# Optimization experiments

Hardware: AMD Instinct MI355X
Metric: run time of the kernel (lower is better)

The kernel has to match this reference:

```python
import jax, jax.numpy as jnp
import numpy as np

N_NODE = 50000
N_EDGE = 800000
D = 64       # in_dim = out_dim = hidden_dim
A = 64       # attn_dim
N_REL = 475  # 2*237+1 relation ids
B = 32       # batch of queries


def setup_inputs() -> dict:
    key = jax.random.key(0)
    ks = jax.random.split(key, 16)
    hidden = jax.random.normal(ks[0], (N_NODE, D), dtype=jnp.float32)
    sub = jax.random.randint(ks[1], (N_EDGE,), 0, N_NODE)
    rel = jax.random.randint(ks[2], (N_EDGE,), 0, N_REL)
    obj = jax.random.randint(ks[3], (N_EDGE,), 0, N_NODE)
    edges = jnp.stack([sub, rel, obj], axis=1)  # [E, 3]
    gnn_emb_rel = jax.random.normal(ks[4], (N_REL, D), dtype=jnp.float32)
    mapping = jax.random.randint(ks[5], (N_REL,), 0, N_REL)  # rel id -> unique-rel row
    q_rel = jax.random.randint(ks[6], (B,), 0, N_REL)
    r_idx = jax.random.randint(ks[7], (N_EDGE,), 0, B)  # edge -> query index
    s = 1.0 / np.sqrt(D)
    sa = 1.0 / np.sqrt(A)
    u = lambda k, shape, b: jax.random.uniform(k, shape, jnp.float32, minval=-b, maxval=b)
    return {
        "hidden": hidden,
        "edges": edges,
        "gnn_emb_rel": gnn_emb_rel,
        "mapping": mapping,
        "q_rel": q_rel,
        "r_idx": r_idx,
        "n_node": N_NODE,
        "Ws_w": u(ks[8], (A, D), s),
        "Wr_w": u(ks[9], (A, D), s),
        "Wqr_w": u(ks[10], (A, D), s),
        "Wqr_b": u(ks[11], (A,), s),
        "walpha_w": u(ks[12], (1, A), sa),
        "walpha_b": u(ks[13], (1,), sa),
        "Wh_w": u(ks[14], (D, D), s),
    }


def reference(hidden, edges, gnn_emb_rel, mapping, q_rel, r_idx, n_node,
              Ws_w, Wr_w, Wqr_w, Wqr_b, walpha_w, walpha_b, Wh_w):
    sub, rel, obj = edges[:, 0], edges[:, 1], edges[:, 2]
    hs = hidden[sub]                       # [E, D] gather
    hr = gnn_emb_rel[mapping[rel]]         # [E, D] gather
    # per-query h_qr projected once, then gathered per edge (same math, cheaper)
    hq = gnn_emb_rel[mapping[q_rel]]       # [B, D]
    qr_attn = hq @ Wqr_w.T + Wqr_b         # [B, A]
    pre = hs @ Ws_w.T + hr @ Wr_w.T + qr_attn[r_idx]   # [E, A]
    alpha = jax.nn.sigmoid(jax.nn.relu(pre) @ walpha_w.T + walpha_b)  # [E, 1]
    message = alpha * (hs * hr)            # [E, D]
    message_agg = jax.ops.segment_sum(message, obj, num_segments=n_node)  # [N, D]
    hidden_new = jax.nn.relu(message_agg @ Wh_w.T)  # act = ReLU from GNN_auto
    return hidden_new
```

## Files before the change

### kernel.cpp

```cpp
#include <hip/hip_runtime.h>
#include <hip/hip_bf16.h>

#define D64 64
#define WTP 65
#define LPAD 68

typedef __attribute__((ext_vector_type(8))) short short8;
typedef __attribute__((ext_vector_type(4))) float f32x4;

__device__ inline float lane_bcast(float v, int l) {
    return __uint_as_float(__builtin_amdgcn_readlane(__float_as_uint(v), l));
}
__device__ inline float bf16_lo(unsigned u) { return __uint_as_float(u << 16); }
__device__ inline float bf16_hi(unsigned u) { return __uint_as_float(u & 0xFFFF0000u); }
__device__ inline float bf16u(unsigned short u) { return __uint_as_float((unsigned)u << 16); }
__device__ inline unsigned short f2bf(float f) {
    __hip_bfloat16 b = __float2bfloat16(f);
    return *(unsigned short*)&b;
}

__global__ void cvtW_kernel(const float* __restrict__ W, unsigned short* __restrict__ WsB) {
    int i = blockIdx.x * blockDim.x + threadIdx.x;
    if (i < D64 * D64) WsB[i] = f2bf(W[i]);
}

__global__ void rowmm_mfma_kernel(const float* __restrict__ in,
                                  const unsigned short* __restrict__ WsB,
                                  unsigned short* __restrict__ outb,
                                  unsigned short* __restrict__ inb, int nrows,
                                  const int* __restrict__ edges, const int* __restrict__ r_idx,
                                  int* __restrict__ counts, uint2* __restrict__ epack, int E) {
    __shared__ unsigned short ldsA[4][16 * LPAD];
    __shared__ unsigned short ldsD[4][16 * LPAD];
    int tid = threadIdx.x;
    int lane = tid & 63;
    int wv = tid >> 6;
    int wid = (blockIdx.x * blockDim.x + tid) >> 6;
    int rbase = wid * 16;

    if (rbase < nrows) {
        short8 bfrag[8];
#pragma unroll
        for (int t = 0; t < 4; ++t)
#pragma unroll
            for (int kk = 0; kk < 2; ++kk)
                bfrag[t * 2 + kk] = *(const short8*)(WsB + (size_t)(t * 16 + (lane & 15)) * D64 +
                                                     kk * 32 + (lane >> 4) * 8);

        unsigned short* la = &ldsA[wv][0];
#pragma unroll
        for (int rr = 0; rr < 16; ++rr) {
            int r = rbase + rr;
            float v = (r < nrows) ? in[(size_t)r * D64 + lane] : 0.f;
            la[rr * LPAD + lane] = f2bf(v);
        }
#pragma unroll
        for (int h = 0; h < 2; ++h) {
            int row = h * 8 + (lane >> 3);
            int col8 = (lane & 7) * 8;
            if (rbase + row < nrows) {
                uint4 v = *(const uint4*)(la + row * LPAD + col8);
                *(uint4*)(inb + (size_t)(rbase + row) * D64 + col8) = v;
            }
        }

        f32x4 acc[4];
#pragma unroll
        for (int t = 0; t < 4; ++t) acc[t] = (f32x4){0.f, 0.f, 0.f, 0.f};
#pragma unroll
        for (int kk = 0; kk < 2; ++kk) {
            short8 afrag = *(const short8*)(la + (lane & 15) * LPAD + kk * 32 + (lane >> 4) * 8);
#pragma unroll
            for (int t = 0; t < 4; ++t)
                acc[t] = __builtin_amdgcn_mfma_f32_16x16x32_bf16(afrag, bfrag[t * 2 + kk],
                                                                 acc[t], 0, 0, 0);
        }
        unsigned short* ld = &ldsD[wv][0];
#pragma unroll
        for (int t = 0; t < 4; ++t)
#pragma unroll
            for (int reg = 0; reg < 4; ++reg)
                ld[((lane >> 4) * 4 + reg) * LPAD + t * 16 + (lane & 15)] = f2bf(acc[t][reg]);
#pragma unroll
        for (int h = 0; h < 2; ++h) {
            int row = h * 8 + (lane >> 3);
            int col8 = (lane & 7) * 8;
            if (rbase + row < nrows) {
                uint4 v = *(const uint4*)(ld + row * LPAD + col8);
                *(uint4*)(outb + (size_t)(rbase + row) * D64 + col8) = v;
            }
        }
    }

    int gt = blockIdx.x * blockDim.x + tid;
    int gs = gridDim.x * blockDim.x;
    for (int i = gt; i < E; i += gs) {
        int sub = edges[i * 3 + 0];
        int rel = edges[i * 3 + 1];
        int obj = edges[i * 3 + 2];
        int ri  = r_idx[i];
        epack[i] = make_uint2((unsigned)sub | ((unsigned)rel << 17) | ((unsigned)ri << 26),
                              (unsigned)obj);
        atomicAdd(&counts[obj], 1);
    }
}

__global__ void prep_kernel(const float* __restrict__ emb, const int* __restrict__ mapping,
                            const int* __restrict__ q_rel,
                            const float* __restrict__ Wr, const float* __restrict__ Wqr,
                            const float* __restrict__ Wqr_b,
                            unsigned short* __restrict__ hrmapb,
                            unsigned short* __restrict__ hrWb,
                            unsigned short* __restrict__ qrb, int nrel, int nq) {
    int b = blockIdx.x;
    int lane = threadIdx.x;
    if (b < nrel) {
        int m = mapping[b];
        float v = emb[m * D64 + lane];
        hrmapb[b * D64 + lane] = f2bf(v);
        float acc = 0.f;
#pragma unroll
        for (int d = 0; d < D64; ++d)
            acc = fmaf(lane_bcast(v, d), Wr[lane * D64 + d], acc);
        hrWb[b * D64 + lane] = f2bf(acc);
    } else {
        int q = b - nrel;
        if (q < nq) {
            int m = mapping[q_rel[q]];
            float v = emb[m * D64 + lane];
            float acc = Wqr_b[lane];
#pragma unroll
            for (int d = 0; d < D64; ++d)
                acc = fmaf(lane_bcast(v, d), Wqr[lane * D64 + d], acc);
            qrb[q * D64 + lane] = f2bf(acc);
        }
    }
}

__global__ void scan1_kernel(const int* __restrict__ counts, int* __restrict__ offs,
                             int* __restrict__ partials, int n) {
    __shared__ int tsum[256];
    int t = threadIdx.x;
    int base = blockIdx.x * 1024 + t * 4;
    int v[4];
    int s = 0;
#pragma unroll
    for (int i = 0; i < 4; ++i) {
        int idx = base + i;
        int c = (idx < n) ? counts[idx] : 0;
        v[i] = s;
        s += c;
    }
    tsum[t] = s;
    __syncthreads();
    for (int off = 1; off < 256; off <<= 1) {
        int y = (t >= off) ? tsum[t - off] : 0;
        __syncthreads();
        tsum[t] += y;
        __syncthreads();
    }
    int incl = tsum[t];
    int thread_prefix = incl - s;
    if (t == 255) partials[blockIdx.x] = incl;
#pragma unroll
    for (int i = 0; i < 4; ++i) {
        int idx = base + i;
        if (idx < n) offs[idx] = thread_prefix + v[i];
    }
}

__global__ void scan2_kernel(int* partials, int nb) {
    int t = threadIdx.x;
    int own = (t < nb) ? partials[t] : 0;
    int v = own;
    for (int off = 1; off < 64; off <<= 1) {
        int y = __shfl_up(v, off, 64);
        if (t >= off) v += y;
    }
    if (t < nb) partials[t] = v - own;
}

__global__ void scan3_kernel(int* __restrict__ offs, const int* __restrict__ partials, int n) {
    int base = blockIdx.x * 1024 + threadIdx.x;
    int add = partials[blockIdx.x];
#pragma unroll
    for (int i = 0; i < 4; ++i) {
        int idx = base + i * 256;
        if (idx < n) offs[idx] += add;
    }
}

__global__ void alpha_scatter_kernel(const uint2* __restrict__ epack,
                                     const unsigned short* __restrict__ hsWb,
                                     const unsigned short* __restrict__ hrWb,
                                     const unsigned short* __restrict__ qrb,
                                     const float* __restrict__ walpha_w,
                                     const float* __restrict__ walpha_b,
                                     int* __restrict__ offs, int2* __restrict__ rec,
                                     int E, int half) {
    int tid = blockIdx.x * blockDim.x + threadIdx.x;
    int e0 = tid >> 3;
    int l = tid & 7;
    if (e0 >= half) return;
    int e1 = e0 + half;
    bool has1 = (e1 < E);

    uint2 p0 = epack[e0];
    uint2 p1 = has1 ? epack[e1] : make_uint2(0u, 0u);
    int sub0 = p0.x & 0x1FFFF, rel0 = (p0.x >> 17) & 0x1FF, ri0 = p0.x >> 26, obj0 = (int)p0.y;
    int sub1 = p1.x & 0x1FFFF, rel1 = (p1.x >> 17) & 0x1FF, ri1 = p1.x >> 26, obj1 = (int)p1.y;

    uint4 hv0 = *(const uint4*)(hsWb + (size_t)sub0 * D64 + l * 8);
    uint4 rv0 = *(const uint4*)(hrWb + (size_t)rel0 * D64 + l * 8);
    uint4 qv0 = *(const uint4*)(qrb  + (size_t)ri0  * D64 + l * 8);
    uint4 hv1 = *(const uint4*)(hsWb + (size_t)sub1 * D64 + l * 8);
    uint4 rv1 = *(const uint4*)(hrWb + (size_t)rel1 * D64 + l * 8);
    uint4 qv1 = *(const uint4*)(qrb  + (size_t)ri1  * D64 + l * 8);
    const float4* w = (const float4*)(walpha_w + l * 8);
    float4 w0 = w[0], w1 = w[1];

    float x0, x1;
    x0 = fmaxf(bf16_lo(hv0.x) + bf16_lo(rv0.x) + bf16_lo(qv0.x), 0.f) * w0.x;
    x0 = fmaf(fmaxf(bf16_hi(hv0.x) + bf16_hi(rv0.x) + bf16_hi(qv0.x), 0.f), w0.y, x0);
    x0 = fmaf(fmaxf(bf16_lo(hv0.y) + bf16_lo(rv0.y) + bf16_lo(qv0.y), 0.f), w0.z, x0);
    x0 = fmaf(fmaxf(bf16_hi(hv0.y) + bf16_hi(rv0.y) + bf16_hi(qv0.y), 0.f), w0.w, x0);
    x0 = fmaf(fmaxf(bf16_lo(hv0.z) + bf16_lo(rv0.z) + bf16_lo(qv0.z), 0.f), w1.x, x0);
    x0 = fmaf(fmaxf(bf16_hi(hv0.z) + bf16_hi(rv0.z) + bf16_hi(qv0.z), 0.f), w1.y, x0);
    x0 = fmaf(fmaxf(bf16_lo(hv0.w) + bf16_lo(rv0.w) + bf16_lo(qv0.w), 0.f), w1.z, x0);
    x0 = fmaf(fmaxf(bf16_hi(hv0.w) + bf16_hi(rv0.w) + bf16_hi(qv0.w), 0.f), w1.w, x0);

    x1 = fmaxf(bf16_lo(hv1.x) + bf16_lo(rv1.x) + bf16_lo(qv1.x), 0.f) * w0.x;
    x1 = fmaf(fmaxf(bf16_hi(hv1.x) + bf16_hi(rv1.x) + bf16_hi(qv1.x), 0.f), w0.y, x1);
    x1 = fmaf(fmaxf(bf16_lo(hv1.y) + bf16_lo(rv1.y) + bf16_lo(qv1.y), 0.f), w0.z, x1);
    x1 = fmaf(fmaxf(bf16_hi(hv1.y) + bf16_hi(rv1.y) + bf16_hi(qv1.y), 0.f), w0.w, x1);
    x1 = fmaf(fmaxf(bf16_lo(hv1.z) + bf16_lo(rv1.z) + bf16_lo(qv1.z), 0.f), w1.x, x1);
    x1 = fmaf(fmaxf(bf16_hi(hv1.z) + bf16_hi(rv1.z) + bf16_hi(qv1.z), 0.f), w1.y, x1);
    x1 = fmaf(fmaxf(bf16_lo(hv1.w) + bf16_lo(rv1.w) + bf16_lo(qv1.w), 0.f), w1.z, x1);
    x1 = fmaf(fmaxf(bf16_hi(hv1.w) + bf16_hi(rv1.w) + bf16_hi(qv1.w), 0.f), w1.w, x1);

    x0 += __shfl_xor(x0, 4, 64);
    x1 += __shfl_xor(x1, 4, 64);
    x0 += __shfl_xor(x0, 2, 64);
    x1 += __shfl_xor(x1, 2, 64);
    x0 += __shfl_xor(x0, 1, 64);
    x1 += __shfl_xor(x1, 1, 64);

    if (l == 0) {
        float wb = walpha_b[0];
        float a0 = 1.f / (1.f + __expf(-(x0 + wb)));
        int slot0 = atomicAdd(&offs[obj0], 1);
        rec[slot0] = make_int2(sub0 | (rel0 << 17), __float_as_int(a0));
        if (has1) {
            float a1 = 1.f / (1.f + __expf(-(x1 + wb)));
            int slot1 = atomicAdd(&offs[obj1], 1);
            rec[slot1] = make_int2(sub1 | (rel1 << 17), __float_as_int(a1));
        }
    }
}

__global__ void agg_wh_kernel(const int2* __restrict__ rec, const int* __restrict__ endoff,
                              const unsigned short* __restrict__ hiddenb,
                              const unsigned short* __restrict__ hrmapb,
                              const float* __restrict__ Wh,
                              float* __restrict__ out, int NN) {
    __shared__ float WT[D64 * WTP];
    int tid = threadIdx.x;
    for (int i = tid; i < D64 * D64; i += blockDim.x)
        WT[(i & 63) * WTP + (i >> 6)] = Wh[i];
    __syncthreads();
    int lane = tid & 63;
    int n = (blockIdx.x * blockDim.x + tid) >> 6;
    if (n >= NN) return;
    int start = (n == 0) ? 0 : endoff[n - 1];
    int end = endoff[n];
    start = __builtin_amdgcn_readfirstlane(start);
    end = __builtin_amdgcn_readfirstlane(end);
    float acc0 = 0.f, acc1 = 0.f, acc2 = 0.f, acc3 = 0.f;
    for (int base = start; base < end; base += 64) {
        int cnt = end - base;
        if (cnt > 64) cnt = 64;
        int rx = 0, ry = 0;
        if (lane < cnt) {
            int2 r = rec[base + lane];
            rx = r.x; ry = r.y;
        }
        int j = 0;
        for (; j + 3 < cnt; j += 4) {
            int rx0 = __builtin_amdgcn_readlane(rx, j);
            int ry0 = __builtin_amdgcn_readlane(ry, j);
            int rx1 = __builtin_amdgcn_readlane(rx, j + 1);
            int ry1 = __builtin_amdgcn_readlane(ry, j + 1);
            int rx2 = __builtin_amdgcn_readlane(rx, j + 2);
            int ry2 = __builtin_amdgcn_readlane(ry, j + 2);
            int rx3 = __builtin_amdgcn_readlane(rx, j + 3);
            int ry3 = __builtin_amdgcn_readlane(ry, j + 3);
            float h0 = bf16u(hiddenb[(size_t)(rx0 & 0x1FFFF) * D64 + lane]);
            float m0 = bf16u(hrmapb[(size_t)((unsigned)rx0 >> 17) * D64 + lane]);
            float h1 = bf16u(hiddenb[(size_t)(rx1 & 0x1FFFF) * D64 + lane]);
            float m1 = bf16u(hrmapb[(size_t)((unsigned)rx1 >> 17) * D64 + lane]);
            float h2 = bf16u(hiddenb[(size_t)(rx2 & 0x1FFFF) * D64 + lane]);
            float m2 = bf16u(hrmapb[(size_t)((unsigned)rx2 >> 17) * D64 + lane]);
            float h3 = bf16u(hiddenb[(size_t)(rx3 & 0x1FFFF) * D64 + lane]);
            float m3 = bf16u(hrmapb[(size_t)((unsigned)rx3 >> 17) * D64 + lane]);
            acc0 = fmaf(__uint_as_float(ry0) * h0, m0, acc0);
            acc1 = fmaf(__uint_as_float(ry1) * h1, m1, acc1);
            acc2 = fmaf(__uint_as_float(ry2) * h2, m2, acc2);
            acc3 = fmaf(__uint_as_float(ry3) * h3, m3, acc3);
        }
        for (; j < cnt; ++j) {
            int rx0 = __builtin_amdgcn_readlane(rx, j);
            int ry0 = __builtin_amdgcn_readlane(ry, j);
            float h0 = bf16u(hiddenb[(size_t)(rx0 & 0x1FFFF) * D64 + lane]);
            float m0 = bf16u(hrmapb[(size_t)((unsigned)rx0 >> 17) * D64 + lane]);
            acc0 = fmaf(__uint_as_float(ry0) * h0, m0, acc0);
        }
    }
    float acc = (acc0 + acc1) + (acc2 + acc3);
    float o = 0.f;
#pragma unroll
    for (int d = 0; d < D64; ++d)
        o = fmaf(lane_bcast(acc, d), WT[d * WTP + lane], o);
    out[(size_t)n * D64 + lane] = fmaxf(o, 0.f);
}

extern "C" void kernel_launch(void* const* d_in, const int* in_sizes, int n_in,
                              void* d_out, int out_size, void* d_ws, size_t ws_size,
                              hipStream_t stream) {
    const float* hidden   = (const float*)d_in[0];
    const int*   edges    = (const int*)d_in[1];
    const float* emb_rel  = (const float*)d_in[2];
    const int*   mapping  = (const int*)d_in[3];
    const int*   q_rel    = (const int*)d_in[4];
    const int*   r_idx    = (const int*)d_in[5];
    const float* Ws_w     = (const float*)d_in[7];
    const float* Wr_w     = (const float*)d_in[8];
    const float* Wqr_w    = (const float*)d_in[9];
    const float* Wqr_b    = (const float*)d_in[10];
    const float* walpha_w = (const float*)d_in[11];
    const float* walpha_b = (const float*)d_in[12];
    const float* Wh_w     = (const float*)d_in[13];
    float* out = (float*)d_out;

    int NN   = in_sizes[0] / D64;
    int E    = in_sizes[5];
    int NREL = in_sizes[3];
    int NQ   = in_sizes[4];

    char* ws = (char*)d_ws;
    size_t off = 0;
    unsigned short* hsWb    = (unsigned short*)(ws + off); off += (size_t)NN * D64 * 2;
    unsigned short* hiddenb = (unsigned short*)(ws + off); off += (size_t)NN * D64 * 2;
    int2*  rec  = (int2*)(ws + off);       off += (size_t)E * sizeof(int2);
    uint2* epack = (uint2*)(ws + off);     off += (size_t)E * sizeof(uint2);
    int* counts = (int*)(ws + off);        off += (size_t)NN * sizeof(int);
    int* offs   = (int*)(ws + off);        off += (size_t)NN * sizeof(int);
    int* partials = (int*)(ws + off);      off += 64 * sizeof(int);
    unsigned short* hrmapb = (unsigned short*)(ws + off); off += (size_t)NREL * D64 * 2;
    unsigned short* hrWb   = (unsigned short*)(ws + off); off += (size_t)NREL * D64 * 2;
    unsigned short* qrb    = (unsigned short*)(ws + off); off += (size_t)NQ * D64 * 2;
    unsigned short* WsB    = (unsigned short*)(ws + off); off += (size_t)D64 * D64 * 2;

    int NB = (NN + 1023) / 1024;

    hipMemsetAsync(counts, 0, (size_t)NN * sizeof(int), stream);
    cvtW_kernel<<<(D64 * D64 + 255) / 256, 256, 0, stream>>>(Ws_w, WsB);
    prep_kernel<<<NREL + NQ, 64, 0, stream>>>(emb_rel, mapping, q_rel, Wr_w, Wqr_w, Wqr_b,
                                              hrmapb, hrWb, qrb, NREL, NQ);
    {
        int waves = (NN + 15) / 16;
        int blocks = (waves * 64 + 255) / 256;
        rowmm_mfma_kernel<<<blocks, 256, 0, stream>>>(hidden, WsB, hsWb, hiddenb, NN,
                                                      edges, r_idx, counts, epack, E);
    }
    scan1_kernel<<<NB, 256, 0, stream>>>(counts, offs, partials, NN);
    scan2_kernel<<<1, 64, 0, stream>>>(partials, NB);
    scan3_kernel<<<NB, 256, 0, stream>>>(offs, partials, NN);
    {
        int half = (E + 1) / 2;
        long long threads = (long long)half * 8;
        int blocks = (int)((threads + 255) / 256);
        alpha_scatter_kernel<<<blocks, 256, 0, stream>>>(epack, hsWb, hrWb, qrb,
                                                         walpha_w, walpha_b, offs, rec, E, half);
    }
    agg_wh_kernel<<<(NN * 64 + 1023) / 1024, 1024, 0, stream>>>(rec, offs, hiddenb, hrmapb,
                                                                Wh_w, out, NN);
}
```

Measured before the change: 154.2 us.

## Merge weight conversion into prep, stage edges in LDS, unroll aggregation gathers by eight

Folds the Ws bf16 conversion into prep_kernel, removing one kernel launch. In the rowmm kernel the LDS staging for the bf16 input copy and the MFMA output is replaced with direct per-element global stores, and edge triples are staged through shared memory so each 256-edge chunk is read coalesced. The aggregation loop gains an 8-way unrolled gather path so more loads are in flight. The trade-off is narrower, non-vectorised global stores in the row matmul and extra barriers in the edge-packing loop.

```diff
diff --git a/kernel.cpp b/kernel.cpp
--- a/kernel.cpp
+++ b/kernel.cpp
@@ -19,9 +19,38 @@
     return *(unsigned short*)&b;
 }
 
-__global__ void cvtW_kernel(const float* __restrict__ W, unsigned short* __restrict__ WsB) {
-    int i = blockIdx.x * blockDim.x + threadIdx.x;
-    if (i < D64 * D64) WsB[i] = f2bf(W[i]);
+__global__ void prep_kernel(const float* __restrict__ emb, const int* __restrict__ mapping,
+                            const int* __restrict__ q_rel,
+                            const float* __restrict__ Wr, const float* __restrict__ Wqr,
+                            const float* __restrict__ Wqr_b, const float* __restrict__ Ws,
+                            unsigned short* __restrict__ hrmapb,
+                            unsigned short* __restrict__ hrWb,
+                            unsigned short* __restrict__ qrb,
+                            unsigned short* __restrict__ WsB, int nrel, int nq) {
+    int b = blockIdx.x;
+    int lane = threadIdx.x;
+    if (b < nrel) {
+        int m = mapping[b];
+        float v = emb[m * D64 + lane];
+        hrmapb[b * D64 + lane] = f2bf(v);
+        float acc = 0.f;
+#pragma unroll
+        for (int d = 0; d < D64; ++d)
+            acc = fmaf(lane_bcast(v, d), Wr[lane * D64 + d], acc);
+        hrWb[b * D64 + lane] = f2bf(acc);
+    } else if (b < nrel + nq) {
+        int q = b - nrel;
+        int m = mapping[q_rel[q]];
+        float v = emb[m * D64 + lane];
+        float acc = Wqr_b[lane];
+#pragma unroll
+        for (int d = 0; d < D64; ++d)
+            acc = fmaf(lane_bcast(v, d), Wqr[lane * D64 + d], acc);
+        qrb[q * D64 + lane] = f2bf(acc);
+    } else {
+        int c = b - nrel - nq;
+        WsB[c * D64 + lane] = f2bf(Ws[c * D64 + lane]);
+    }
 }
 
 __global__ void rowmm_mfma_kernel(const float* __restrict__ in,
@@ -31,7 +60,7 @@
                                   const int* __restrict__ edges, const int* __restrict__ r_idx,
                                   int* __restrict__ counts, uint2* __restrict__ epack, int E) {
     __shared__ unsigned short ldsA[4][16 * LPAD];
-    __shared__ unsigned short ldsD[4][16 * LPAD];
+    __shared__ int eStage[768];
     int tid = threadIdx.x;
     int lane = tid & 63;
     int wv = tid >> 6;
@@ -52,16 +81,9 @@
         for (int rr = 0; rr < 16; ++rr) {
             int r = rbase + rr;
             float v = (r < nrows) ? in[(size_t)r * D64 + lane] : 0.f;
-            la[rr * LPAD + lane] = f2bf(v);
-        }
-#pragma unroll
-        for (int h = 0; h < 2; ++h) {
-            int row = h * 8 + (lane >> 3);
-            int col8 = (lane & 7) * 8;
-            if (rbase + row < nrows) {
-                uint4 v = *(const uint4*)(la + row * LPAD + col8);
-                *(uint4*)(inb + (size_t)(rbase + row) * D64 + col8) = v;
-            }
+            unsigned short bb = f2bf(v);
+            if (r < nrows) inb[(size_t)r * D64 + lane] = bb;
+            la[rr * LPAD + lane] = bb;
         }
 
         f32x4 acc[4];
@@ -75,64 +97,34 @@
                 acc[t] = __builtin_amdgcn_mfma_f32_16x16x32_bf16(afrag, bfrag[t * 2 + kk],
                                                                  acc[t], 0, 0, 0);
         }
-        unsigned short* ld = &ldsD[wv][0];
 #pragma unroll
         for (int t = 0; t < 4; ++t)
 #pragma unroll
-            for (int reg = 0; reg < 4; ++reg)
-                ld[((lane >> 4) * 4 + reg) * LPAD + t * 16 + (lane & 15)] = f2bf(acc[t][reg]);
-#pragma unroll
-        for (int h = 0; h < 2; ++h) {
-            int row = h * 8 + (lane >> 3);
-            int col8 = (lane & 7) * 8;
-            if (rbase + row < nrows) {
-                uint4 v = *(const uint4*)(ld + row * LPAD + col8);
-                *(uint4*)(outb + (size_t)(rbase + row) * D64 + col8) = v;
+            for (int reg = 0; reg < 4; ++reg) {
+                int row = rbase + (lane >> 4) * 4 + reg;
+                int col = t * 16 + (lane & 15);
+                if (row < nrows)
+                    outb[(size_t)row * D64 + col] = f2bf(acc[t][reg]);
             }
-        }
-    }
-
-    int gt = blockIdx.x * blockDim.x + tid;
-    int gs = gridDim.x * blockDim.x;
-    for (int i = gt; i < E; i += gs) {
-        int sub = edges[i * 3 + 0];
-        int rel = edges[i * 3 + 1];
-        int obj = edges[i * 3 + 2];
-        int ri  = r_idx[i];
-        epack[i] = make_uint2((unsigned)sub | ((unsigned)rel << 17) | ((unsigned)ri << 26),
-                              (unsigned)obj);
-        atomicAdd(&counts[obj], 1);
-    }
-}
-
-__global__ void prep_kernel(const float* __restrict__ emb, const int* __restrict__ mapping,
-                            const int* __restrict__ q_rel,
-                            const float* __restrict__ Wr, const float* __restrict__ Wqr,
-                            const float* __restrict__ Wqr_b,
-                            unsigned short* __restrict__ hrmapb,
-                            unsigned short* __restrict__ hrWb,
-                            unsigned short* __restrict__ qrb, int nrel, int nq) {
-    int b = blockIdx.x;
-    int lane = threadIdx.x;
-    if (b < nrel) {
-        int m = mapping[b];
-        float v = emb[m * D64 + lane];
-        hrmapb[b * D64 + lane] = f2bf(v);
-        float acc = 0.f;
-#pragma unroll
-        for (int d = 0; d < D64; ++d)
-            acc = fmaf(lane_bcast(v, d), Wr[lane * D64 + d], acc);
-        hrWb[b * D64 + lane] = f2bf(acc);
-    } else {
-        int q = b - nrel;
-        if (q < nq) {
-            int m = mapping[q_rel[q]];
-            float v = emb[m * D64 + lane];
-            float acc = Wqr_b[lane];
-#pragma unroll
-            for (int d = 0; d < D64; ++d)
-                acc = fmaf(lane_bcast(v, d), Wqr[lane * D64 + d], acc);
-            qrb[q * D64 + lane] = f2bf(acc);
+    }
+
+    int nChunks = (E + 255) / 256;
+    for (int chunk = blockIdx.x; chunk < nChunks; chunk += gridDim.x) {
+        int base = chunk * 256;
+        int cnt = min(256, E - base);
+        __syncthreads();
+        for (int k = tid; k < cnt * 3; k += 256)
+            eStage[k] = edges[(size_t)base * 3 + k];
+        __syncthreads();
+        if (tid < cnt) {
+            int i = base + tid;
+            int sub = eStage[tid * 3 + 0];
+            int rel = eStage[tid * 3 + 1];
+            int obj = eStage[tid * 3 + 2];
+            int ri  = r_idx[i];
+            epack[i] = make_uint2((unsigned)sub | ((unsigned)rel << 17) | ((unsigned)ri << 26),
+                                  (unsigned)obj);
+            atomicAdd(&counts[obj], 1);
         }
     }
 }
@@ -285,6 +277,28 @@
             rx = r.x; ry = r.y;
         }
         int j = 0;
+        for (; j + 7 < cnt; j += 8) {
+            int a_rx[8], a_ry[8];
+#pragma unroll
+            for (int k = 0; k < 8; ++k) {
+                a_rx[k] = __builtin_amdgcn_readlane(rx, j + k);
+                a_ry[k] = __builtin_amdgcn_readlane(ry, j + k);
+            }
+            float h[8], m[8];
+#pragma unroll
+            for (int k = 0; k < 8; ++k) {
+                h[k] = bf16u(hiddenb[(size_t)(a_rx[k] & 0x1FFFF) * D64 + lane]);
+                m[k] = bf16u(hrmapb[(size_t)((unsigned)a_rx[k] >> 17) * D64 + lane]);
+            }
+            acc0 = fmaf(__uint_as_float(a_ry[0]) * h[0], m[0], acc0);
+            acc1 = fmaf(__uint_as_float(a_ry[1]) * h[1], m[1], acc1);
+            acc2 = fmaf(__uint_as_float(a_ry[2]) * h[2], m[2], acc2);
+            acc3 = fmaf(__uint_as_float(a_ry[3]) * h[3], m[3], acc3);
+            acc0 = fmaf(__uint_as_float(a_ry[4]) * h[4], m[4], acc0);
+            acc1 = fmaf(__uint_as_float(a_ry[5]) * h[5], m[5], acc1);
+            acc2 = fmaf(__uint_as_float(a_ry[6]) * h[6], m[6], acc2);
+            acc3 = fmaf(__uint_as_float(a_ry[7]) * h[7], m[7], acc3);
+        }
         for (; j + 3 < cnt; j += 4) {
             int rx0 = __builtin_amdgcn_readlane(rx, j);
             int ry0 = __builtin_amdgcn_readlane(ry, j);
@@ -363,9 +377,9 @@
     int NB = (NN + 1023) / 1024;
 
     hipMemsetAsync(counts, 0, (size_t)NN * sizeof(int), stream);
-    cvtW_kernel<<<(D64 * D64 + 255) / 256, 256, 0, stream>>>(Ws_w, WsB);
-    prep_kernel<<<NREL + NQ, 64, 0, stream>>>(emb_rel, mapping, q_rel, Wr_w, Wqr_w, Wqr_b,
-                                              hrmapb, hrWb, qrb, NREL, NQ);
+    prep_kernel<<<NREL + NQ + 64, 64, 0, stream>>>(emb_rel, mapping, q_rel, Wr_w, Wqr_w,
+                                                   Wqr_b, Ws_w, hrmapb, hrWb, qrb, WsB,
+                                                   NREL, NQ);
     {
         int waves = (NN + 15) / 16;
         int blocks = (waves * 64 + 255) / 256;
```

Result: faster. 150.7 us (-2.3%).
